# Performance work log

Hardware: AMD Instinct MI355X
Metric: run time of the kernel (lower is better)

## Reference

```python
import jax, jax.numpy as jnp
import numpy as np

B = 128        # graphs
N_PER = 1024   # nodes per graph
K = 7          # knn neighbors
X_SIZE = 16
POS_SIZE = 3
H1, H2 = 64, 128
N = B * N_PER
EPS = 1e-5


def _lin_init(key, din, dout):
    kw, kb = jax.random.split(key)
    s = 1.0 / np.sqrt(din)
    w = jax.random.uniform(kw, (din, dout), jnp.float32, -s, s)
    b = jax.random.uniform(kb, (dout,), jnp.float32, -s, s)
    return w, b


def setup_inputs() -> dict:
    key = jax.random.key(0)
    ks = jax.random.split(key, 12)
    x = jax.random.normal(ks[0], (N, X_SIZE), jnp.float32)
    pos = jax.random.normal(ks[1], (N, POS_SIZE), jnp.float32)
    batch = jnp.repeat(jnp.arange(B, dtype=jnp.int32), N_PER)
    wk1, bk1 = _lin_init(ks[2], X_SIZE, H1)
    wq1, bq1 = _lin_init(ks[3], X_SIZE, H1)
    wv1, bv1 = _lin_init(ks[4], X_SIZE, H1)
    ws1, bs1 = _lin_init(ks[5], X_SIZE, H1)
    wk2, bk2 = _lin_init(ks[6], H1, H2)
    wq2, bq2 = _lin_init(ks[7], H1, H2)
    wv2, bv2 = _lin_init(ks[8], H1, H2)
    ws2, bs2 = _lin_init(ks[9], H1, H2)
    g1 = jnp.ones((H1,), jnp.float32); be1 = jnp.zeros((H1,), jnp.float32)
    g2 = jnp.ones((H2,), jnp.float32); be2 = jnp.zeros((H2,), jnp.float32)
    return dict(x=x, pos=pos, batch=batch,
                wk1=wk1, bk1=bk1, wq1=wq1, bq1=bq1, wv1=wv1, bv1=bv1, ws1=ws1, bs1=bs1, g1=g1, be1=be1,
                wk2=wk2, bk2=bk2, wq2=wq2, bq2=bq2, wv2=wv2, bv2=bv2, ws2=ws2, bs2=bs2, g2=g2, be2=be2)


def knn_edges(pos):
    # batch-aware kNN: graphs are equal-sized contiguous blocks of N_PER nodes
    p = pos.reshape(B, N_PER, POS_SIZE)
    def per_graph(pg):
        d = jnp.sum((pg[:, None, :] - pg[None, :, :]) ** 2, axis=-1)  # [n, n]
        d = jnp.where(jnp.eye(N_PER, dtype=bool), jnp.inf, d)          # no self loops
        _, idx = jax.lax.top_k(-d, K)                                   # [n, K]
        return idx
    idx = jax.vmap(per_graph)(p)                       # [B, N_PER, K]
    offs = (jnp.arange(B) * N_PER)[:, None, None]
    src = (idx + offs).reshape(-1)                     # neighbor j (source)
    dst = jnp.broadcast_to(jnp.arange(N_PER)[None, :, None] + offs, (B, N_PER, K)).reshape(-1)
    return src, dst


def res_gated_conv(x, src, dst, wk, bk, wq, bq, wv, bv, ws, bs):
    # out_i = skip(x_i) + sum_{j->i} sigmoid(K x_i + Q x_j) * V x_j
    kf = x @ wk + bk
    qf = x @ wq + bq
    vf = x @ wv + bv
    msg = jax.nn.sigmoid(kf[dst] + qf[src]) * vf[src]  # [E, out]
    agg = jnp.zeros_like(kf).at[dst].add(msg)
    return agg + x @ ws + bs


def batch_norm(x, gamma, beta):
    m = x.mean(0)
    v = jnp.mean((x - m) ** 2, 0)  # biased var (training-mode BN)
    return (x - m) * jax.lax.rsqrt(v + EPS) * gamma + beta


def reference(x, pos, batch, wk1, bk1, wq1, bq1, wv1, bv1, ws1, bs1, g1, be1,
              wk2, bk2, wq2, bq2, wv2, bv2, ws2, bs2, g2, be2):
    src, dst = knn_edges(pos)
    h = jax.nn.relu(batch_norm(res_gated_conv(x, src, dst, wk1, bk1, wq1, bq1, wv1, bv1, ws1, bs1), g1, be1))
    h = jax.nn.relu(batch_norm(res_gated_conv(h, src, dst, wk2, bk2, wq2, bq2, wv2, bv2, ws2, bs2), g2, be2))
    s = jax.ops.segment_sum(h, batch, num_segments=B)
    cnt = jax.ops.segment_sum(jnp.ones((h.shape[0], 1), h.dtype), batch, num_segments=B)
    return s / cnt
```

## Files before the change

kernel.cpp:

```cpp
#include <hip/hip_runtime.h>
#include <hip/hip_bf16.h>

#define BGR   128
#define NPER  1024
#define NK    7
#define NNODES (BGR*NPER)

typedef __attribute__((ext_vector_type(8))) short short8;
typedef __attribute__((ext_vector_type(8))) unsigned short ushort8;
typedef __attribute__((ext_vector_type(4))) float floatx4;

static __device__ __forceinline__ float bf2f(unsigned short u) {
    unsigned int x = ((unsigned int)u) << 16;
    return __builtin_bit_cast(float, x);
}
static __device__ __forceinline__ unsigned short f2bf(float f) {
    unsigned int x = __builtin_bit_cast(unsigned int, f);
    unsigned int lsb = (x >> 16) & 1u;
    x += 0x7fffu + lsb;
    return (unsigned short)(x >> 16);
}
static __device__ __forceinline__ float packdi(float d, int j) {
    unsigned int ub = (__builtin_bit_cast(unsigned int, d) & 0xFFFFFC00u) | (unsigned int)j;
    return __builtin_bit_cast(float, ub);
}

__global__ __launch_bounds__(256) void knn_kernel(const float* __restrict__ pos,
                                                  int* __restrict__ idx) {
    __shared__ __align__(16) floatx4 sp[NPER + 1];
    int g     = blockIdx.x >> 2;
    int qbase = (blockIdx.x & 3) << 8;
    int base  = g * NPER;
    const float* pg = pos + (size_t)base * 3;
    for (int t = threadIdx.x; t < NPER * 3; t += 256) {
        float v = pg[t];
        int j = t / 3, comp = t - j * 3;
        int slot = j + (j >= 512 ? 1 : 0);
        ((float*)&sp[slot])[comp] = v;
    }
    __syncthreads();
    for (int j = threadIdx.x; j < NPER; j += 256) {
        int slot = j + (j >= 512 ? 1 : 0);
        floatx4 q = sp[slot];
        sp[slot].w = fmaf(q.x, q.x, fmaf(q.y, q.y, q.z * q.z));
    }
    __syncthreads();

    int lane = threadIdx.x & 63;
    int wv   = (int)threadIdx.x >> 6;
    int p    = lane >> 1;
    int hf   = lane & 1;
    int qA   = qbase + wv * 64 + 2 * p;
    int qB   = qA + 1;
    floatx4 meA = sp[qA + (qA >= 512 ? 1 : 0)];
    floatx4 meB = sp[qB + (qB >= 512 ? 1 : 0)];
    float mAx = -2.f * meA.x, mAy = -2.f * meA.y, mAz = -2.f * meA.z;
    float mBx = -2.f * meB.x, mBy = -2.f * meB.y, mBz = -2.f * meB.z;
    const floatx4* cp = sp + hf;

    float a0=3e38f,a1=3e38f,a2=3e38f,a3=3e38f,a4=3e38f,a5=3e38f,a6=3e38f,a7=3e38f;
    float c0=3e38f,c1=3e38f,c2=3e38f,c3=3e38f,c4=3e38f,c5=3e38f,c6=3e38f,c7=3e38f;
    int j0base = hf << 9;
    for (int j0 = j0base; j0 < j0base + 512; j0 += 8) {
        #pragma unroll
        for (int u = 0; u < 8; ++u) {
            floatx4 q = cp[j0 + u];
            float dA = fmaf(mAx, q.x, fmaf(mAy, q.y, fmaf(mAz, q.z, q.w)));
            float dB = fmaf(mBx, q.x, fmaf(mBy, q.y, fmaf(mBz, q.z, q.w)));
            float tA = packdi(dA, j0 + u);
            float tB = packdi(dB, j0 + u);
            float nA7 = __builtin_amdgcn_fmed3f(a6, a7, tA);
            float nA6 = __builtin_amdgcn_fmed3f(a5, a6, tA);
            float nA5 = __builtin_amdgcn_fmed3f(a4, a5, tA);
            float nA4 = __builtin_amdgcn_fmed3f(a3, a4, tA);
            float nA3 = __builtin_amdgcn_fmed3f(a2, a3, tA);
            float nA2 = __builtin_amdgcn_fmed3f(a1, a2, tA);
            float nA1 = __builtin_amdgcn_fmed3f(a0, a1, tA);
            a0 = fminf(a0, tA);
            a1 = nA1; a2 = nA2; a3 = nA3; a4 = nA4; a5 = nA5; a6 = nA6; a7 = nA7;
            float nB7 = __builtin_amdgcn_fmed3f(c6, c7, tB);
            float nB6 = __builtin_amdgcn_fmed3f(c5, c6, tB);
            float nB5 = __builtin_amdgcn_fmed3f(c4, c5, tB);
            float nB4 = __builtin_amdgcn_fmed3f(c3, c4, tB);
            float nB3 = __builtin_amdgcn_fmed3f(c2, c3, tB);
            float nB2 = __builtin_amdgcn_fmed3f(c1, c2, tB);
            float nB1 = __builtin_amdgcn_fmed3f(c0, c1, tB);
            c0 = fminf(c0, tB);
            c1 = nB1; c2 = nB2; c3 = nB3; c4 = nB4; c5 = nB5; c6 = nB6; c7 = nB7;
        }
    }
    bool ev = (hf == 0);
    float x0 = ev ? c0 : a0, x1 = ev ? c1 : a1, x2 = ev ? c2 : a2, x3 = ev ? c3 : a3,
          x4 = ev ? c4 : a4, x5 = ev ? c5 : a5, x6 = ev ? c6 : a6, x7 = ev ? c7 : a7;
    float o0 = __shfl_xor(x0, 1), o1 = __shfl_xor(x1, 1), o2 = __shfl_xor(x2, 1),
          o3 = __shfl_xor(x3, 1), o4 = __shfl_xor(x4, 1), o5 = __shfl_xor(x5, 1),
          o6 = __shfl_xor(x6, 1), o7 = __shfl_xor(x7, 1);
    float m0 = ev ? a0 : c0, m1 = ev ? a1 : c1, m2 = ev ? a2 : c2, m3 = ev ? a3 : c3,
          m4 = ev ? a4 : c4, m5 = ev ? a5 : c5, m6 = ev ? a6 : c6, m7 = ev ? a7 : c7;
    int qm = qA + hf;
    bool sm = ((qm >> 9) == hf);
    float A1 = sm ? m1 : o1, A2 = sm ? m2 : o2, A3 = sm ? m3 : o3, A4 = sm ? m4 : o4,
          A5 = sm ? m5 : o5, A6 = sm ? m6 : o6, A7 = sm ? m7 : o7;
    float B0 = sm ? o0 : m0, B1 = sm ? o1 : m1, B2 = sm ? o2 : m2, B3 = sm ? o3 : m3,
          B4 = sm ? o4 : m4, B5 = sm ? o5 : m5, B6 = sm ? o6 : m6;
    int4 r0, r1;
    r0.x = base + (int)(__builtin_bit_cast(unsigned int, fminf(A1, B6)) & 1023u);
    r0.y = base + (int)(__builtin_bit_cast(unsigned int, fminf(A2, B5)) & 1023u);
    r0.z = base + (int)(__builtin_bit_cast(unsigned int, fminf(A3, B4)) & 1023u);
    r0.w = base + (int)(__builtin_bit_cast(unsigned int, fminf(A4, B3)) & 1023u);
    r1.x = base + (int)(__builtin_bit_cast(unsigned int, fminf(A5, B2)) & 1023u);
    r1.y = base + (int)(__builtin_bit_cast(unsigned int, fminf(A6, B1)) & 1023u);
    r1.z = base + (int)(__builtin_bit_cast(unsigned int, fminf(A7, B0)) & 1023u);
    r1.w = base;
    int4* op = (int4*)(idx + (size_t)(base + qm) * 8);
    op[0] = r0;
    op[1] = r1;
}

__global__ __launch_bounds__(256) void feat1_kernel(
    const float* __restrict__ x,
    const float* __restrict__ wk, const float* __restrict__ bk,
    const float* __restrict__ wq, const float* __restrict__ bq,
    const float* __restrict__ wv, const float* __restrict__ bv,
    const float* __restrict__ wsm, const float* __restrict__ bs,
    unsigned int* __restrict__ qv, unsigned int* __restrict__ ks) {
    int c = threadIdx.x & 63;
    float Wk[16], Wq[16], Wv[16], Ws[16];
    #pragma unroll
    for (int k = 0; k < 16; ++k) {
        Wk[k] = wk[k*64+c]; Wq[k] = wq[k*64+c]; Wv[k] = wv[k*64+c]; Ws[k] = wsm[k*64+c];
    }
    float Bk = bk[c], Bq = bq[c], Bv = bv[c], Bs = bs[c];
    int wave = blockIdx.x * (blockDim.x >> 6) + (threadIdx.x >> 6);
    int nw   = gridDim.x * (blockDim.x >> 6);
    for (int n = wave; n < NNODES; n += nw) {
        const float* xr = x + (size_t)n * 16;
        float ak = Bk, aq = Bq, av = Bv, as = Bs;
        #pragma unroll
        for (int k = 0; k < 16; ++k) {
            float xv = xr[k];
            ak += xv * Wk[k]; aq += xv * Wq[k]; av += xv * Wv[k]; as += xv * Ws[k];
        }
        size_t o = (size_t)n * 64 + c;
        qv[o] = ((unsigned int)f2bf(av) << 16) | f2bf(aq);
        ks[o] = ((unsigned int)f2bf(as) << 16) | f2bf(ak);
    }
}

template<int C>
__global__ __launch_bounds__(256) void conv_kernel(
    const unsigned int* __restrict__ qv, const unsigned int* __restrict__ ks,
    const int* __restrict__ idx, unsigned short* __restrict__ h,
    float* __restrict__ part) {
    const int NPB = 256 / C;
    int c   = threadIdx.x & (C - 1);
    int sub = __builtin_amdgcn_readfirstlane((int)(threadIdx.x / C));
    int b     = blockIdx.x;
    int xcd   = b & 7;
    int chunk = b >> 3;
    int graph = xcd * 16 + (chunk >> 5);
    int nblk  = chunk & 31;
    int n0 = graph * NPER + nblk * 32;
    float s = 0.f, s2 = 0.f;
    #pragma unroll 4
    for (int i = sub; i < 32; i += NPB) {
        int n = n0 + i;
        const int4* nb4 = (const int4*)(idx + (size_t)n * 8);
        int4 na = nb4[0];
        int4 nbv = nb4[1];
        unsigned int ku = ks[(size_t)n * C + c];
        float kv  = bf2f((unsigned short)(ku & 0xFFFF));
        float acc = bf2f((unsigned short)(ku >> 16));
        int jj[7] = {na.x, na.y, na.z, na.w, nbv.x, nbv.y, nbv.z};
        #pragma unroll
        for (int k = 0; k < NK; ++k) {
            int j = __builtin_amdgcn_readfirstlane(jj[k]);
            const unsigned int* p = qv + (size_t)j * C;
            unsigned int u = p[c];
            float qvv = bf2f((unsigned short)(u & 0xFFFF));
            float vvv = bf2f((unsigned short)(u >> 16));
            float t = kv + qvv;
            float sg = __builtin_amdgcn_rcpf(1.f + __expf(-t));
            acc = fmaf(sg, vvv, acc);
        }
        unsigned short hb = f2bf(acc);
        h[(size_t)n * C + c] = hb;
        float hv = bf2f(hb);
        s += hv; s2 += hv * hv;
    }
    __shared__ float ls[256], ls2[256];
    ls[threadIdx.x] = s; ls2[threadIdx.x] = s2;
    __syncthreads();
    if (threadIdx.x < C) {
        #pragma unroll
        for (int l = 1; l < NPB; ++l) { s += ls[threadIdx.x + l*C]; s2 += ls2[threadIdx.x + l*C]; }
        part[(size_t)blockIdx.x * 2 * C + threadIdx.x]     = s;
        part[(size_t)blockIdx.x * 2 * C + C + threadIdx.x] = s2;
    }
}

template<int C>
static __device__ __forceinline__ void bnfin_body(
    const float* __restrict__ part, const float* __restrict__ gamma,
    const float* __restrict__ beta, float* __restrict__ ss,
    int c, float* ls, float* ls2) {
    float s = 0.f, s2 = 0.f;
    for (int b = threadIdx.x; b < 4096; b += 256) {
        s  += part[(size_t)b * 2 * C + c];
        s2 += part[(size_t)b * 2 * C + C + c];
    }
    ls[threadIdx.x] = s; ls2[threadIdx.x] = s2;
    __syncthreads();
    for (int st = 128; st > 0; st >>= 1) {
        if (threadIdx.x < st) { ls[threadIdx.x] += ls[threadIdx.x+st]; ls2[threadIdx.x] += ls2[threadIdx.x+st]; }
        __syncthreads();
    }
    if (threadIdx.x == 0) {
        float m   = ls[0] / (float)NNODES;
        float var = ls2[0] / (float)NNODES - m * m;
        float inv = rsqrtf(var + 1e-5f);
        float sc  = gamma[c] * inv;
        ss[c]     = sc;
        ss[C + c] = beta[c] - m * sc;
    }
}

template<int C>
__global__ __launch_bounds__(256) void bnfin_kernel(
    const float* __restrict__ part, const float* __restrict__ gamma,
    const float* __restrict__ beta, float* __restrict__ ss) {
    __shared__ float ls[256], ls2[256];
    bnfin_body<C>(part, gamma, beta, ss, blockIdx.x, ls, ls2);
}

__global__ __launch_bounds__(256) void fin1_wfrag_kernel(
    const float* __restrict__ part, const float* __restrict__ gamma,
    const float* __restrict__ beta, float* __restrict__ ss,
    const float* __restrict__ w0, const float* __restrict__ w1,
    const float* __restrict__ w2, const float* __restrict__ w3,
    unsigned short* __restrict__ frag) {
    __shared__ float ls[256], ls2[256];
    if (blockIdx.x < 64) {
        bnfin_body<64>(part, gamma, beta, ss, blockIdx.x, ls, ls2);
        return;
    }
    int s  = blockIdx.x - 64;
    if (threadIdx.x >= 64) return;
    int m  = s >> 4;
    int kt = (s >> 3) & 1;
    int ct = s & 7;
    const float* w = (m == 0) ? w0 : (m == 1) ? w1 : (m == 2) ? w2 : w3;
    int l = threadIdx.x;
    int col = ct * 16 + (l & 15);
    int kbase = kt * 32 + (l >> 4) * 8;
    unsigned short* out = frag + ((size_t)s * 64 + l) * 8;
    #pragma unroll
    for (int e = 0; e < 8; ++e) out[e] = f2bf(w[(size_t)(kbase + e) * 128 + col]);
}

__global__ __launch_bounds__(256) void feat2_kernel(
    const unsigned short* __restrict__ h1n, const unsigned short* __restrict__ frag,
    const float* __restrict__ ss1,
    const float* __restrict__ b0, const float* __restrict__ b1,
    const float* __restrict__ b2, const float* __restrict__ b3,
    unsigned int* __restrict__ qv2, unsigned int* __restrict__ ks2) {
    __shared__ unsigned short xh[2][2][16][17];
    int nt = blockIdx.x;
    int m  = threadIdx.x >> 6;
    int l  = threadIdx.x & 63;
    const float* bm = (m == 0) ? b0 : (m == 1) ? b1 : (m == 2) ? b2 : b3;
    int lr = l & 15;
    int gq = l >> 4;
    int n  = nt * 16 + lr;
    const unsigned short* ar = h1n + (size_t)n * 64 + gq * 8;
    short8 a0r = *(const short8*)ar;
    short8 a1r = *(const short8*)(ar + 32);
    short8 a0, a1;
    #pragma unroll
    for (int e = 0; e < 8; ++e) {
        int c0 = gq * 8 + e;
        float f0 = bf2f((unsigned short)a0r[e]) * ss1[c0] + ss1[64 + c0];
        a0[e] = (short)f2bf(fmaxf(f0, 0.f));
        int c1 = 32 + gq * 8 + e;
        float f1 = bf2f((unsigned short)a1r[e]) * ss1[c1] + ss1[64 + c1];
        a1[e] = (short)f2bf(fmaxf(f1, 0.f));
    }
    #pragma unroll
    for (int ct = 0; ct < 8; ++ct) {
        size_t fb0 = ((size_t)(m * 16 + ct)     * 64 + l) * 8;
        size_t fb1 = ((size_t)(m * 16 + 8 + ct) * 64 + l) * 8;
        short8 w0 = *(const short8*)(frag + fb0);
        short8 w1 = *(const short8*)(frag + fb1);
        float bv = bm[ct * 16 + lr];
        floatx4 acc = {bv, bv, bv, bv};
        acc = __builtin_amdgcn_mfma_f32_16x16x32_bf16(a0, w0, acc, 0, 0, 0);
        acc = __builtin_amdgcn_mfma_f32_16x16x32_bf16(a1, w1, acc, 0, 0, 0);
        if (m >= 2) {
            #pragma unroll
            for (int r = 0; r < 4; ++r)
                xh[ct & 1][m - 2][gq * 4 + r][lr] = f2bf(acc[r]);
        }
        __syncthreads();
        if (m < 2) {
            unsigned int* od = (m == 1) ? qv2 : ks2;
            int set = (m == 1) ? 0 : 1;
            #pragma unroll
            for (int r = 0; r < 4; ++r) {
                unsigned int lo = f2bf(acc[r]);
                unsigned int hi = xh[ct & 1][set][gq * 4 + r][lr];
                od[(size_t)(nt * 16 + gq * 4 + r) * 128 + ct * 16 + lr] = (hi << 16) | lo;
            }
        }
    }
}

__global__ __launch_bounds__(256) void pool_partial_kernel(const unsigned short* __restrict__ h2,
                                                           const float* __restrict__ ss2,
                                                           float* __restrict__ part) {
    int g = blockIdx.x >> 3;
    int q = blockIdx.x & 7;
    int c = threadIdx.x & 127;
    int isub = threadIdx.x >> 7;
    float sc = ss2[c], sh = ss2[128 + c];
    float acc = 0.f;
    const unsigned short* hp = h2 + ((size_t)g * NPER + q * 128) * 128;
    for (int i = isub; i < 128; i += 2)
        acc += fmaxf(bf2f(hp[(size_t)i * 128 + c]) * sc + sh, 0.f);
    __shared__ float red[256];
    red[threadIdx.x] = acc;
    __syncthreads();
    if (threadIdx.x < 128)
        part[(size_t)blockIdx.x * 128 + c] = acc + red[threadIdx.x + 128];
}

__global__ void pool_final_kernel(const float* __restrict__ part, float* __restrict__ out) {
    int g = blockIdx.x, c = threadIdx.x;
    float s = 0.f;
    #pragma unroll
    for (int q = 0; q < 8; ++q) s += part[(size_t)(g * 8 + q) * 128 + c];
    out[(size_t)g * 128 + c] = s * (1.f / 1024.f);
}

extern "C" void kernel_launch(void* const* d_in, const int* in_sizes, int n_in,
                              void* d_out, int out_size, void* d_ws, size_t ws_size,
                              hipStream_t stream) {
    const float* x   = (const float*)d_in[0];
    const float* pos = (const float*)d_in[1];
    const float* wk1 = (const float*)d_in[3];
    const float* bk1 = (const float*)d_in[4];
    const float* wq1 = (const float*)d_in[5];
    const float* bq1 = (const float*)d_in[6];
    const float* wv1 = (const float*)d_in[7];
    const float* bv1 = (const float*)d_in[8];
    const float* ws1 = (const float*)d_in[9];
    const float* bs1 = (const float*)d_in[10];
    const float* g1  = (const float*)d_in[11];
    const float* be1 = (const float*)d_in[12];
    const float* wk2 = (const float*)d_in[13];
    const float* bk2 = (const float*)d_in[14];
    const float* wq2 = (const float*)d_in[15];
    const float* bq2 = (const float*)d_in[16];
    const float* wv2 = (const float*)d_in[17];
    const float* bv2 = (const float*)d_in[18];
    const float* ws2 = (const float*)d_in[19];
    const float* bs2 = (const float*)d_in[20];
    const float* g2  = (const float*)d_in[21];
    const float* be2 = (const float*)d_in[22];
    float* out = (float*)d_out;

    const size_t SZ_QV1 = (size_t)NNODES * 64 * 4;
    const size_t SZ_QV2 = (size_t)NNODES * 128 * 4;

    char* ws = (char*)d_ws;
    size_t off = 0;
    auto alloc = [&](size_t b) { size_t o = off; off += (b + 255) & ~(size_t)255; return o; };

    int* idx              = (int*)(ws + alloc((size_t)NNODES * 8 * 4));
    size_t o_region       = alloc(2 * SZ_QV2);
    unsigned int* qv1     = (unsigned int*)(ws + o_region);
    unsigned int* ks1     = (unsigned int*)(ws + o_region + SZ_QV1);
    unsigned int* qv2     = (unsigned int*)(ws + o_region);
    unsigned int* ks2     = (unsigned int*)(ws + o_region + SZ_QV2);
    unsigned short* h1    = (unsigned short*)(ws + alloc((size_t)NNODES * 64 * 2));
    unsigned short* h2    = (unsigned short*)(ws + alloc((size_t)NNODES * 128 * 2));
    unsigned short* frag  = (unsigned short*)(ws + alloc(64 * 64 * 8 * 2));
    float* part           = (float*)(ws + alloc((size_t)4096 * 2 * 128 * 4));
    float* ss1            = (float*)(ws + alloc(2 * 64 * 4));
    float* ss2            = (float*)(ws + alloc(2 * 128 * 4));
    (void)ws_size; (void)in_sizes; (void)n_in; (void)out_size;

    knn_kernel<<<BGR * 4, 256, 0, stream>>>(pos, idx);
    feat1_kernel<<<1024, 256, 0, stream>>>(x, wk1, bk1, wq1, bq1, wv1, bv1, ws1, bs1,
                                           qv1, ks1);
    conv_kernel<64><<<NNODES / 32, 256, 0, stream>>>(qv1, ks1, idx, h1, part);
    fin1_wfrag_kernel<<<128, 256, 0, stream>>>(part, g1, be1, ss1,
                                               wk2, wq2, wv2, ws2, frag);
    feat2_kernel<<<NNODES / 16, 256, 0, stream>>>(h1, frag, ss1, bk2, bq2, bv2, bs2,
                                                  qv2, ks2);
    conv_kernel<128><<<NNODES / 32, 256, 0, stream>>>(qv2, ks2, idx, h2, part);
    bnfin_kernel<128><<<128, 256, 0, stream>>>(part, g2, be2, ss2);
    pool_partial_kernel<<<BGR * 8, 256, 0, stream>>>(h2, ss2, part);
    pool_final_kernel<<<BGR, 128, 0, stream>>>(part, out);
}
```

Baseline: 244.9 us.

## Split kNN candidate scan across eight lanes with butterfly bitonic merges

Each query pair's 1024 candidates are now split across 8 lanes of 128 each, instead of 2 lanes of 512. The per-lane top-8 lists are combined with xor-shuffle bitonic merges, and the grid grows fourfold so each block handles 64 queries. The shared-memory layout is padded per 128-candidate segment to avoid bank conflicts. This shortens each thread's serial insertion chain and raises occupancy and latency hiding, at the cost of each block reloading all positions and doing extra shuffle and merge work.

```diff
diff --git a/kernel.cpp b/kernel.cpp
--- a/kernel.cpp
+++ b/kernel.cpp
@@ -27,20 +27,20 @@
 
 __global__ __launch_bounds__(256) void knn_kernel(const float* __restrict__ pos,
                                                   int* __restrict__ idx) {
-    __shared__ __align__(16) floatx4 sp[NPER + 1];
-    int g     = blockIdx.x >> 2;
-    int qbase = (blockIdx.x & 3) << 8;
+    __shared__ __align__(16) floatx4 sp[8 * 129];
+    int g     = blockIdx.x >> 4;
+    int qbase = (blockIdx.x & 15) << 6;
     int base  = g * NPER;
     const float* pg = pos + (size_t)base * 3;
     for (int t = threadIdx.x; t < NPER * 3; t += 256) {
         float v = pg[t];
         int j = t / 3, comp = t - j * 3;
-        int slot = j + (j >= 512 ? 1 : 0);
+        int slot = (j >> 7) * 129 + (j & 127);
         ((float*)&sp[slot])[comp] = v;
     }
     __syncthreads();
     for (int j = threadIdx.x; j < NPER; j += 256) {
-        int slot = j + (j >= 512 ? 1 : 0);
+        int slot = (j >> 7) * 129 + (j & 127);
         floatx4 q = sp[slot];
         sp[slot].w = fmaf(q.x, q.x, fmaf(q.y, q.y, q.z * q.z));
     }
@@ -48,27 +48,27 @@
 
     int lane = threadIdx.x & 63;
     int wv   = (int)threadIdx.x >> 6;
-    int p    = lane >> 1;
-    int hf   = lane & 1;
-    int qA   = qbase + wv * 64 + 2 * p;
-    int qB   = qA + 1;
-    floatx4 meA = sp[qA + (qA >= 512 ? 1 : 0)];
-    floatx4 meB = sp[qB + (qB >= 512 ? 1 : 0)];
+    int grp  = lane >> 3;
+    int e    = lane & 7;
+    int qA_l = qbase + (wv * 8 + grp) * 2;
+    int qB_l = qA_l + 1;
+    floatx4 meA = sp[(qA_l >> 7) * 129 + (qA_l & 127)];
+    floatx4 meB = sp[(qB_l >> 7) * 129 + (qB_l & 127)];
     float mAx = -2.f * meA.x, mAy = -2.f * meA.y, mAz = -2.f * meA.z;
     float mBx = -2.f * meB.x, mBy = -2.f * meB.y, mBz = -2.f * meB.z;
-    const floatx4* cp = sp + hf;
+    const floatx4* cp = sp + e * 129;
+    int jbase = e << 7;
 
     float a0=3e38f,a1=3e38f,a2=3e38f,a3=3e38f,a4=3e38f,a5=3e38f,a6=3e38f,a7=3e38f;
     float c0=3e38f,c1=3e38f,c2=3e38f,c3=3e38f,c4=3e38f,c5=3e38f,c6=3e38f,c7=3e38f;
-    int j0base = hf << 9;
-    for (int j0 = j0base; j0 < j0base + 512; j0 += 8) {
-        #pragma unroll
-        for (int u = 0; u < 8; ++u) {
-            floatx4 q = cp[j0 + u];
+    for (int jp = 0; jp < 128; jp += 4) {
+        #pragma unroll
+        for (int u = 0; u < 4; ++u) {
+            floatx4 q = cp[jp + u];
             float dA = fmaf(mAx, q.x, fmaf(mAy, q.y, fmaf(mAz, q.z, q.w)));
             float dB = fmaf(mBx, q.x, fmaf(mBy, q.y, fmaf(mBz, q.z, q.w)));
-            float tA = packdi(dA, j0 + u);
-            float tB = packdi(dB, j0 + u);
+            float tA = packdi(dA, jbase + jp + u);
+            float tB = packdi(dB, jbase + jp + u);
             float nA7 = __builtin_amdgcn_fmed3f(a6, a7, tA);
             float nA6 = __builtin_amdgcn_fmed3f(a5, a6, tA);
             float nA5 = __builtin_amdgcn_fmed3f(a4, a5, tA);
@@ -89,32 +89,52 @@
             c1 = nB1; c2 = nB2; c3 = nB3; c4 = nB4; c5 = nB5; c6 = nB6; c7 = nB7;
         }
     }
-    bool ev = (hf == 0);
-    float x0 = ev ? c0 : a0, x1 = ev ? c1 : a1, x2 = ev ? c2 : a2, x3 = ev ? c3 : a3,
-          x4 = ev ? c4 : a4, x5 = ev ? c5 : a5, x6 = ev ? c6 : a6, x7 = ev ? c7 : a7;
-    float o0 = __shfl_xor(x0, 1), o1 = __shfl_xor(x1, 1), o2 = __shfl_xor(x2, 1),
-          o3 = __shfl_xor(x3, 1), o4 = __shfl_xor(x4, 1), o5 = __shfl_xor(x5, 1),
-          o6 = __shfl_xor(x6, 1), o7 = __shfl_xor(x7, 1);
-    float m0 = ev ? a0 : c0, m1 = ev ? a1 : c1, m2 = ev ? a2 : c2, m3 = ev ? a3 : c3,
-          m4 = ev ? a4 : c4, m5 = ev ? a5 : c5, m6 = ev ? a6 : c6, m7 = ev ? a7 : c7;
-    int qm = qA + hf;
-    bool sm = ((qm >> 9) == hf);
-    float A1 = sm ? m1 : o1, A2 = sm ? m2 : o2, A3 = sm ? m3 : o3, A4 = sm ? m4 : o4,
-          A5 = sm ? m5 : o5, A6 = sm ? m6 : o6, A7 = sm ? m7 : o7;
-    float B0 = sm ? o0 : m0, B1 = sm ? o1 : m1, B2 = sm ? o2 : m2, B3 = sm ? o3 : m3,
-          B4 = sm ? o4 : m4, B5 = sm ? o5 : m5, B6 = sm ? o6 : m6;
-    int4 r0, r1;
-    r0.x = base + (int)(__builtin_bit_cast(unsigned int, fminf(A1, B6)) & 1023u);
-    r0.y = base + (int)(__builtin_bit_cast(unsigned int, fminf(A2, B5)) & 1023u);
-    r0.z = base + (int)(__builtin_bit_cast(unsigned int, fminf(A3, B4)) & 1023u);
-    r0.w = base + (int)(__builtin_bit_cast(unsigned int, fminf(A4, B3)) & 1023u);
-    r1.x = base + (int)(__builtin_bit_cast(unsigned int, fminf(A5, B2)) & 1023u);
-    r1.y = base + (int)(__builtin_bit_cast(unsigned int, fminf(A6, B1)) & 1023u);
-    r1.z = base + (int)(__builtin_bit_cast(unsigned int, fminf(A7, B0)) & 1023u);
-    r1.w = base;
-    int4* op = (int4*)(idx + (size_t)(base + qm) * 8);
-    op[0] = r0;
-    op[1] = r1;
+
+    float A[8] = {a0,a1,a2,a3,a4,a5,a6,a7};
+    float C[8] = {c0,c1,c2,c3,c4,c5,c6,c7};
+    #pragma unroll
+    for (int st = 0; st < 2; ++st) {
+        int mask = 1 << st;
+        #pragma unroll
+        for (int ch = 0; ch < 2; ++ch) {
+            float* L = ch ? C : A;
+            float B[8], T[8];
+            #pragma unroll
+            for (int i = 0; i < 8; ++i) B[i] = __shfl_xor(L[i], mask);
+            #pragma unroll
+            for (int i = 0; i < 8; ++i) T[i] = fminf(L[i], B[7 - i]);
+            #define CEx(x,y) { float mn = fminf(T[x], T[y]); float mx = fmaxf(T[x], T[y]); T[x] = mn; T[y] = mx; }
+            CEx(0,4) CEx(1,5) CEx(2,6) CEx(3,7)
+            CEx(0,2) CEx(1,3) CEx(4,6) CEx(5,7)
+            CEx(0,1) CEx(2,3) CEx(4,5) CEx(6,7)
+            #undef CEx
+            #pragma unroll
+            for (int i = 0; i < 8; ++i) L[i] = T[i];
+        }
+    }
+    float OA[8], OC[8];
+    #pragma unroll
+    for (int i = 0; i < 8; ++i) { OA[i] = __shfl_xor(A[i], 4); OC[i] = __shfl_xor(C[i], 4); }
+
+    if (e < 2) {
+        float *M, *O;
+        int qm_l;
+        if (e == 0) { M = A;  O = OA; qm_l = qA_l; }
+        else        { M = C;  O = OC; qm_l = qB_l; }
+        bool selfInM = (qm_l >> 9) == 0;
+        int r[7];
+        #pragma unroll
+        for (int i = 0; i < 7; ++i) {
+            float mm = selfInM ? fminf(M[i + 1], O[6 - i]) : fminf(O[i + 1], M[6 - i]);
+            r[i] = base + (int)(__builtin_bit_cast(unsigned int, mm) & 1023u);
+        }
+        int4* op = (int4*)(idx + (size_t)(base + qm_l) * 8);
+        int4 r0, r1;
+        r0.x = r[0]; r0.y = r[1]; r0.z = r[2]; r0.w = r[3];
+        r1.x = r[4]; r1.y = r[5]; r1.z = r[6]; r1.w = base;
+        op[0] = r0;
+        op[1] = r1;
+    }
 }
 
 __global__ __launch_bounds__(256) void feat1_kernel(
@@ -389,7 +409,7 @@
     float* ss2            = (float*)(ws + alloc(2 * 128 * 4));
     (void)ws_size; (void)in_sizes; (void)n_in; (void)out_size;
 
-    knn_kernel<<<BGR * 4, 256, 0, stream>>>(pos, idx);
+    knn_kernel<<<BGR * 16, 256, 0, stream>>>(pos, idx);
     feat1_kernel<<<1024, 256, 0, stream>>>(x, wk1, bk1, wq1, bq1, wv1, bv1, ws1, bs1,
                                            qv1, ks1);
     conv_kernel<64><<<NNODES / 32, 256, 0, stream>>>(qv1, ks1, idx, h1, part);
```

Result: no change. 243.1 us (-0.8%).
